# Kernel tuning notes

Hardware: AMD Instinct MI355X
Metric: run time of the kernel (lower is better)

The kernel has to match this reference:

```python
import jax, jax.numpy as jnp
import numpy as np

N = 100000
E = 1600000
D_IN = 128
D_H = 128


def _logit(p):
    p = max(min(p, 0.999), 0.001)
    return float(np.log(p / (1.0 - p)))


def setup_inputs() -> dict:
    key = jax.random.key(0)
    ks = jax.random.split(key, 16)
    s = 0.05
    inp = {
        "x": jax.random.normal(ks[0], (N, D_IN), jnp.float32),
        "edge_index": jax.random.randint(ks[1], (2, E), 0, N, jnp.int64),
        "reranker_scores": jax.random.normal(ks[2], (N,), jnp.float32),
        # input_proj
        "Wp": jax.random.normal(ks[3], (D_IN, D_H), jnp.float32) * s,
        "bp": jnp.zeros((D_H,), jnp.float32),
        # SAGEConv 0: lin_l (on aggregated neighbors, has bias), lin_r (root, no bias)
        "Wl0": jax.random.normal(ks[4], (D_IN, D_H), jnp.float32) * s,
        "bl0": jnp.zeros((D_H,), jnp.float32),
        "Wr0": jax.random.normal(ks[5], (D_IN, D_H), jnp.float32) * s,
        # SAGEConv 1
        "Wl1": jax.random.normal(ks[6], (D_H, D_H), jnp.float32) * s,
        "bl1": jnp.zeros((D_H,), jnp.float32),
        "Wr1": jax.random.normal(ks[7], (D_H, D_H), jnp.float32) * s,
        # score head: Linear(128,64) -> GELU -> Linear(64,1)
        "Ws1": jax.random.normal(ks[8], (D_H, D_H // 2), jnp.float32) * s,
        "bs1": jnp.zeros((D_H // 2,), jnp.float32),
        "Ws2": jax.random.normal(ks[9], (D_H // 2, 1), jnp.float32) * s,
        "bs2": jnp.zeros((1,), jnp.float32),
        "alpha_logit": jnp.asarray(_logit(0.65), jnp.float32),
    }
    return inp


def _sage(h, src, dst, Wl, bl, Wr):
    # PyG SAGEConv (aggr='mean'): lin_l(mean_{j in N(i)} x_j) + lin_r(x_i)
    agg = jax.ops.segment_sum(h[src], dst, num_segments=N)  # [N, d]
    deg = jax.ops.segment_sum(jnp.ones((src.shape[0],), h.dtype), dst, num_segments=N)
    mean = agg / jnp.maximum(deg, 1.0)[:, None]
    return mean @ Wl + bl + h @ Wr


def reference(x, edge_index, reranker_scores, Wp, bp, Wl0, bl0, Wr0, Wl1, bl1, Wr1,
              Ws1, bs1, Ws2, bs2, alpha_logit):
    src, dst = edge_index[0], edge_index[1]
    gelu = lambda t: jax.nn.gelu(t, approximate=False)  # torch nn.GELU default = exact erf
    residual = x @ Wp + bp
    # layer 0 (dropout inactive at eval)
    h = gelu(_sage(x, src, dst, Wl0, bl0, Wr0)) + residual
    # layer 1
    h = gelu(_sage(h, src, dst, Wl1, bl1, Wr1)) + h
    gnn_scores = (gelu(h @ Ws1 + bs1) @ Ws2 + bs2)[:, 0]  # [N]
    alpha = jax.nn.sigmoid(alpha_logit)
    return alpha * reranker_scores + (1.0 - alpha) * gnn_scores
```

## Files before the change

kernel.cpp:

```cpp
#include <hip/hip_runtime.h>

typedef unsigned short u16;
typedef unsigned char  u8;
typedef unsigned int   u32;
typedef unsigned long long u64;
typedef __attribute__((ext_vector_type(8))) short short8;
typedef __attribute__((ext_vector_type(4))) float f32x4;
typedef __attribute__((ext_vector_type(2))) float f32x2;

#define PIN8(v) asm volatile("" : "+v"(v))

__device__ __forceinline__ float b2f(u16 u) { return __uint_as_float(((u32)u) << 16); }
__device__ __forceinline__ u16 f2b(float f) {
    u32 i = __float_as_uint(f);
    return (u16)((i + 0x7FFFu + ((i >> 16) & 1u)) >> 16);
}
__device__ __forceinline__ float gelu_f(float v) {
    return 0.5f * v * (1.f + erff(v * 0.70710678118654752f));
}
__device__ __forceinline__ float ldf(const void* p, int i, int f32) {
    return f32 ? ((const float*)p)[i] : b2f(((const u16*)p)[i]);
}

__device__ __forceinline__ float fp8_dec(u32 v) {
    u32 bits = ((v & 0x80u) << 24) | ((v & 0x7Fu) << 20);
    return __uint_as_float(bits) * 1.3292279957849159e36f;
}
__device__ __forceinline__ u32 fp8_enc(float x) {
    u32 b = __float_as_uint(x);
    u32 s = (b >> 24) & 0x80u;
    float ax = fminf(__uint_as_float(b & 0x7FFFFFFFu), 448.f);
    u32 r;
    if (ax < 0.015625f) {
        r = (u32)(ax * 512.f + 0.5f);
    } else {
        u32 ab = __float_as_uint(ax);
        u32 rb = ab + 0x7FFFFu + ((ab >> 20) & 1u);
        int e8 = (int)(rb >> 23) - 120;
        u32 m = (rb >> 20) & 7u;
        if (e8 > 15) { e8 = 15; m = 6u; }
        r = ((u32)e8 << 3) | m;
    }
    return s | r;
}

__device__ __forceinline__ f32x2 dec2_fp8(u32 v) {
#if __has_builtin(__builtin_amdgcn_cvt_pk_f32_fp8)
    return __builtin_amdgcn_cvt_pk_f32_fp8((int)v, false);
#else
    f32x2 r; r[0] = fp8_dec(v); r[1] = fp8_dec(v >> 8); return r;
#endif
}
__device__ __forceinline__ u32 pk4_fp8(float v0, float v1, float v2, float v3) {
#if __has_builtin(__builtin_amdgcn_cvt_pk_fp8_f32)
    int p = __builtin_amdgcn_cvt_pk_fp8_f32(v0, v1, 0, false);
    p = __builtin_amdgcn_cvt_pk_fp8_f32(v2, v3, p, true);
    return (u32)p;
#else
    return fp8_enc(v0) | (fp8_enc(v1) << 8) | (fp8_enc(v2) << 16) | (fp8_enc(v3) << 24);
#endif
}

__global__ void probe_kernel(const int* __restrict__ ei, const u16* __restrict__ xw,
                             int* __restrict__ mode) {
    int lane = threadIdx.x;
    int v = (lane < 8) ? ei[2 * lane + 1] : 0;
    unsigned long long nz = __ballot(v != 0);
    u16 h = xw[2 * lane];
    int e = (h >> 7) & 0xFF;
    unsigned long long pl = __ballot(e >= 100 && e <= 140);
    if (lane == 0) {
        mode[0] = (nz == 0ULL) ? 1 : 0;
        mode[1] = (__popcll(pl) >= 48) ? 0 : 1;
    }
}

__global__ __launch_bounds__(256) void fallback_kernel(const void* __restrict__ rr,
                                                       const void* __restrict__ al,
                                                       const int* __restrict__ mode,
                                                       void* __restrict__ out, int N) {
    int i = blockIdx.x * 256 + threadIdx.x;
    if (i >= N) return;
    int f32 = mode ? mode[1] : 0;
    float a = 1.f / (1.f + expf(-ldf(al, 0, f32)));
    float v = a * ldf(rr, i, f32);
    if (f32) ((float*)out)[i] = v; else ((u16*)out)[i] = f2b(v);
}

__global__ __launch_bounds__(256) void hist_kernel(const int* __restrict__ ei, int E, int N,
                                                   const int* __restrict__ mode,
                                                   int* __restrict__ deg) {
    int i = blockIdx.x * 256 + threadIdx.x;
    if (i >= E) return;
    int m64 = mode[0];
    int d = m64 ? ei[2 * E + 2 * i] : ei[E + i];
    if ((unsigned)d < (unsigned)N) atomicAdd(&deg[d], 1);
}

__global__ __launch_bounds__(256) void bucketHist2_kernel(const int* __restrict__ ei, int E, int N,
                                                          const int* __restrict__ mode, int shift,
                                                          int* __restrict__ chist, int chunks) {
    __shared__ int h[1024];
    int t = threadIdx.x;
#pragma unroll
    for (int j = 0; j < 4; j++) h[t + j * 256] = 0;
    __syncthreads();
    const int m64 = mode[0];
    const int base = blockIdx.x * 2048;
#pragma unroll
    for (int j = 0; j < 8; j++) {
        int i = base + j * 256 + t;
        if (i < E) {
            int d = m64 ? ei[2 * E + 2 * i] : ei[E + i];
            if ((unsigned)d < (unsigned)N) atomicAdd(&h[d >> shift], 1);
        }
    }
    __syncthreads();
#pragma unroll
    for (int j = 0; j < 4; j++) {
        int b = t + j * 256;
        chist[(size_t)b * chunks + blockIdx.x] = h[b];
    }
}

__global__ __launch_bounds__(256) void scanA_kernel(const int* __restrict__ deg,
                                                    int* __restrict__ part) {
    int t = threadIdx.x, lane = t & 63, wv = t >> 6;
    size_t base = (size_t)blockIdx.x * 2048 + (size_t)t * 8;
    int s = 0;
#pragma unroll
    for (int j = 0; j < 8; j++) s += deg[base + j];
    for (int m = 1; m < 64; m <<= 1) s += __shfl_xor(s, m, 64);
    __shared__ int ws4[4];
    if (lane == 0) ws4[wv] = s;
    __syncthreads();
    if (t == 0) part[blockIdx.x] = ws4[0] + ws4[1] + ws4[2] + ws4[3];
}

__global__ void scanB_kernel(int* __restrict__ part, int nb) {
    int lane = threadIdx.x;
    int v = (lane < nb) ? part[lane] : 0;
    int orig = v;
    for (int d = 1; d < 64; d <<= 1) {
        int o = __shfl_up(v, d, 64);
        if (lane >= d) v += o;
    }
    if (lane < nb) part[lane] = v - orig;
}

__global__ __launch_bounds__(256) void scanC_kernel(const int* __restrict__ deg,
                                                    const int* __restrict__ part,
                                                    int* __restrict__ off) {
    int t = threadIdx.x, lane = t & 63, wv = t >> 6;
    size_t base = (size_t)blockIdx.x * 2048 + (size_t)t * 8;
    int v[8];
    int s = 0;
#pragma unroll
    for (int j = 0; j < 8; j++) { v[j] = deg[base + j]; s += v[j]; }
    int incl = s;
    for (int d = 1; d < 64; d <<= 1) {
        int o = __shfl_up(incl, d, 64);
        if (lane >= d) incl += o;
    }
    __shared__ int wsum[4];
    if (lane == 63) wsum[wv] = incl;
    __syncthreads();
    int pre = part[blockIdx.x] + (incl - s);
    for (int w = 0; w < wv; w++) pre += wsum[w];
#pragma unroll
    for (int j = 0; j < 8; j++) { off[base + j] = pre; pre += v[j]; }
    if (blockIdx.x == gridDim.x - 1 && t == 255) off[base + 8] = pre;
}

__global__ __launch_bounds__(256) void scanK_kernel(const int* __restrict__ bcnt,
                                                    int* __restrict__ boff) {
    int t = threadIdx.x, lane = t & 63, wv = t >> 6;
    int v[4];
    int s = 0;
#pragma unroll
    for (int j = 0; j < 4; j++) { v[j] = bcnt[t * 4 + j]; s += v[j]; }
    int incl = s;
    for (int d = 1; d < 64; d <<= 1) {
        int o = __shfl_up(incl, d, 64);
        if (lane >= d) incl += o;
    }
    __shared__ int wsum[4];
    if (lane == 63) wsum[wv] = incl;
    __syncthreads();
    int pre = incl - s;
    for (int w = 0; w < wv; w++) pre += wsum[w];
#pragma unroll
    for (int j = 0; j < 4; j++) { boff[t * 4 + j] = pre; pre += v[j]; }
    if (t == 255) boff[1024] = pre;
}

__global__ __launch_bounds__(256) void chunkScanPre_kernel(int* __restrict__ chist,
                                                           int* __restrict__ bcnt, int chunks) {
    const int b = (blockIdx.x * 256 + threadIdx.x) >> 6;
    if (b >= 1024) return;
    const int lane = threadIdx.x & 63;
    const int per = (chunks + 63) >> 6;
    int* row = chist + (size_t)b * chunks;
    int v[32];
    int sum = 0;
#pragma unroll
    for (int j = 0; j < 32; j++) {
        int c = lane * per + j;
        v[j] = (j < per && c < chunks) ? row[c] : 0;
        sum += v[j];
    }
    int pre = sum;
    for (int d = 1; d < 64; d <<= 1) {
        int o = __shfl_up(pre, d, 64);
        if (lane >= d) pre += o;
    }
    if (lane == 63) bcnt[b] = pre;
    pre -= sum;
#pragma unroll
    for (int j = 0; j < 32; j++) {
        int c = lane * per + j;
        if (j < per && c < chunks) { row[c] = pre; pre += v[j]; }
    }
}

__global__ __launch_bounds__(256) void bucketScatter2_kernel(const int* __restrict__ ei, int E, int N,
                                                             const int* __restrict__ mode, int shift,
                                                             const int* __restrict__ cbase,
                                                             const int* __restrict__ boff,
                                                             u64* __restrict__ pairs, int chunks) {
    __shared__ int cur[1024];
    int t = threadIdx.x;
#pragma unroll
    for (int j = 0; j < 4; j++) {
        int b = t + j * 256;
        cur[b] = cbase[(size_t)b * chunks + blockIdx.x] + boff[b];
    }
    __syncthreads();
    const int m64 = mode[0];
    const int base = blockIdx.x * 2048;
#pragma unroll
    for (int j = 0; j < 8; j++) {
        int i = base + j * 256 + t;
        if (i < E) {
            int d = m64 ? ei[2 * E + 2 * i] : ei[E + i];
            if ((unsigned)d >= (unsigned)N) continue;
            int s = m64 ? ei[2 * i] : ei[i];
            if ((unsigned)s >= (unsigned)N) s = 0;
            int p = atomicAdd(&cur[d >> shift], 1);
            pairs[p] = ((u64)(u32)d << 32) | (u32)s;
        }
    }
}

__global__ __launch_bounds__(256) void bucketFill2_kernel(const u64* __restrict__ pairs,
                                                          const int* __restrict__ boff,
                                                          int* __restrict__ off,
                                                          int* __restrict__ sorted,
                                                          int shift, int E, int N) {
    __shared__ int cur[2048];
    __shared__ int wsum[4];
    const int b = blockIdx.x;
    const int t = threadIdx.x;
    const int lane = t & 63, wv = t >> 6;
    const int nodes = 1 << shift;
    const int nbase = b << shift;
    for (int i = t; i < nodes; i += 256) cur[i] = 0;
    __syncthreads();
    const int s0 = boff[b], s1 = boff[b + 1];
    for (int i = s0 + t; i < s1; i += 256) {
        int li = (int)(pairs[i] >> 32) - nbase;
        if ((unsigned)li < (unsigned)nodes) atomicAdd(&cur[li], 1);
    }
    __syncthreads();
    const int per = (nodes + 255) >> 8;
    int v[8];
    int sum = 0;
#pragma unroll
    for (int j = 0; j < 8; j++) {
        int idx = t * per + j;
        v[j] = (j < per && idx < nodes) ? cur[idx] : 0;
        sum += v[j];
    }
    int incl = sum;
    for (int d = 1; d < 64; d <<= 1) {
        int o = __shfl_up(incl, d, 64);
        if (lane >= d) incl += o;
    }
    if (lane == 63) wsum[wv] = incl;
    __syncthreads();
    int pre = s0 + (incl - sum);
    for (int w = 0; w < wv; w++) pre += wsum[w];
#pragma unroll
    for (int j = 0; j < 8; j++) {
        int idx = t * per + j;
        if (j < per && idx < nodes) {
            cur[idx] = pre;
            if (nbase + idx <= N) off[nbase + idx] = pre;
            pre += v[j];
        }
    }
    if (t == 255 && nbase + nodes <= N) off[nbase + nodes] = s1;
    __syncthreads();
    for (int i = s0 + t; i < s1; i += 256) {
        u64 pr = pairs[i];
        int li = (int)(pr >> 32) - nbase;
        if ((unsigned)li >= (unsigned)nodes) continue;
        int p = atomicAdd(&cur[li], 1);
        if ((unsigned)p < (unsigned)E) sorted[p] = (int)(u32)pr;
    }
}

__global__ __launch_bounds__(256) void fill_kernel(const int* __restrict__ ei, int E, int N,
                                                   const int* __restrict__ mode,
                                                   const int* __restrict__ off,
                                                   int* __restrict__ deg,
                                                   int* __restrict__ sorted) {
    int i = blockIdx.x * 256 + threadIdx.x;
    if (i >= E) return;
    int m64 = mode[0];
    int s = m64 ? ei[2 * i] : ei[i];
    int d = m64 ? ei[2 * E + 2 * i] : ei[E + i];
    if ((unsigned)d >= (unsigned)N) return;
    if ((unsigned)s >= (unsigned)N) s = 0;
    int p = atomicSub(&deg[d], 1) - 1;
    if (p < 0) return;
    int pos = off[d] + p;
    if ((unsigned)pos < (unsigned)E) sorted[pos] = s;
}

__global__ __launch_bounds__(256) void prep_kernel(const void* __restrict__ Wp, const void* __restrict__ Wl0,
                                                   const void* __restrict__ Wr0, const void* __restrict__ Wl1,
                                                   const void* __restrict__ Wr1, const void* __restrict__ Ws1,
                                                   const int* __restrict__ mode, u16* __restrict__ T) {
    int idx = blockIdx.x * 256 + threadIdx.x;
    int f32 = mode[1];
    if (idx < 81920) {
        int m = idx >> 14, e = idx & 16383, n = e & 127, k = e >> 7;
        const void* s;
        switch (m) {
            case 0: s = Wp; break;
            case 1: s = Wl0; break;
            case 2: s = Wr0; break;
            case 3: s = Wl1; break;
            default: s = Wr1; break;
        }
        T[m * 16384 + n * 128 + k] = f2b(ldf(s, e, f32));
    } else if (idx < 90112) {
        int e = idx - 81920, k = e >> 6, n = e & 63;
        T[81920 + n * 128 + k] = f2b(ldf(Ws1, e, f32));
    }
}

template <int F32>
__global__ __launch_bounds__(256) void cvt8_kernel(const void* __restrict__ H, u8* __restrict__ F,
                                                   const int* __restrict__ mode, int NE, int checkMode) {
    if (checkMode && mode[1] != F32) return;
    int i = blockIdx.x * 256 + threadIdx.x;
    if (i >= NE) return;
    float x0, x1;
    if (!F32) {
        u32 v = ((const u32*)H)[i];
        x0 = b2f((u16)v); x1 = b2f((u16)(v >> 16));
    } else {
        x0 = ((const float*)H)[2 * i]; x1 = ((const float*)H)[2 * i + 1];
    }
#if __has_builtin(__builtin_amdgcn_cvt_pk_fp8_f32)
    ((u16*)F)[i] = (u16)__builtin_amdgcn_cvt_pk_fp8_f32(x0, x1, 0, false);
#else
    ((u16*)F)[i] = (u16)(fp8_enc(x0) | (fp8_enc(x1) << 8));
#endif
}

__global__ __launch_bounds__(256) void sagg8_kernel(const u8* __restrict__ F, const int* __restrict__ off,
                                                    const int* __restrict__ srcs, u16* __restrict__ meanO,
                                                    int N, int E) {
    const int node = __builtin_amdgcn_readfirstlane(blockIdx.x * 4 + (threadIdx.x >> 6));
    if (node >= N) return;
    const int lane = threadIdx.x & 63;
    int s0 = off[node], s1 = off[node + 1];
    if (s0 < 0) s0 = 0;
    if (s1 > E) s1 = E;
    if (s1 < s0) s1 = s0;
    const int dg = s1 - s0;
    const float inv = 1.f / (float)(dg > 1 ? dg : 1);
    const u8* Fp = F + lane * 2;
    float a0 = 0.f, a1 = 0.f;
    for (int base = s0; base < s1; base += 64) {
        const int rem = s1 - base;
        const int cnt = rem < 64 ? rem : 64;
        int msrc = srcs[base + (lane < cnt ? lane : 0)];
        if ((unsigned)msrc >= (unsigned)N) msrc = 0;
        int e = 0;
        for (; e + 7 < cnt; e += 8) {
            int i0 = __shfl(msrc, e + 0, 64);
            int i1 = __shfl(msrc, e + 1, 64);
            int i2 = __shfl(msrc, e + 2, 64);
            int i3 = __shfl(msrc, e + 3, 64);
            int i4 = __shfl(msrc, e + 4, 64);
            int i5 = __shfl(msrc, e + 5, 64);
            int i6 = __shfl(msrc, e + 6, 64);
            int i7 = __shfl(msrc, e + 7, 64);
            u32 v0 = *(const u16*)(Fp + (size_t)i0 * 128);
            u32 v1 = *(const u16*)(Fp + (size_t)i1 * 128);
            u32 v2 = *(const u16*)(Fp + (size_t)i2 * 128);
            u32 v3 = *(const u16*)(Fp + (size_t)i3 * 128);
            u32 v4 = *(const u16*)(Fp + (size_t)i4 * 128);
            u32 v5 = *(const u16*)(Fp + (size_t)i5 * 128);
            u32 v6 = *(const u16*)(Fp + (size_t)i6 * 128);
            u32 v7 = *(const u16*)(Fp + (size_t)i7 * 128);
            f32x2 d0 = dec2_fp8(v0), d1 = dec2_fp8(v1), d2 = dec2_fp8(v2), d3 = dec2_fp8(v3);
            f32x2 d4 = dec2_fp8(v4), d5 = dec2_fp8(v5), d6 = dec2_fp8(v6), d7 = dec2_fp8(v7);
            a0 += (d0[0] + d1[0]) + (d2[0] + d3[0]) + (d4[0] + d5[0]) + (d6[0] + d7[0]);
            a1 += (d0[1] + d1[1]) + (d2[1] + d3[1]) + (d4[1] + d5[1]) + (d6[1] + d7[1]);
        }
        for (; e + 3 < cnt; e += 4) {
            int i0 = __shfl(msrc, e + 0, 64);
            int i1 = __shfl(msrc, e + 1, 64);
            int i2 = __shfl(msrc, e + 2, 64);
            int i3 = __shfl(msrc, e + 3, 64);
            u32 v0 = *(const u16*)(Fp + (size_t)i0 * 128);
            u32 v1 = *(const u16*)(Fp + (size_t)i1 * 128);
            u32 v2 = *(const u16*)(Fp + (size_t)i2 * 128);
            u32 v3 = *(const u16*)(Fp + (size_t)i3 * 128);
            f32x2 d0 = dec2_fp8(v0), d1 = dec2_fp8(v1), d2 = dec2_fp8(v2), d3 = dec2_fp8(v3);
            a0 += (d0[0] + d1[0]) + (d2[0] + d3[0]);
            a1 += (d0[1] + d1[1]) + (d2[1] + d3[1]);
        }
        for (; e < cnt; ++e) {
            int i0 = __shfl(msrc, e, 64);
            f32x2 d0 = dec2_fp8(*(const u16*)(Fp + (size_t)i0 * 128));
            a0 += d0[0];
            a1 += d0[1];
        }
    }
    *(u32*)(meanO + (size_t)node * 128 + lane * 2) = (u32)f2b(a0 * inv) | ((u32)f2b(a1 * inv) << 16);
}

template <int F32>
__global__ __launch_bounds__(256) void saggb_kernel(const void* __restrict__ H, const int* __restrict__ off,
                                                    const int* __restrict__ srcs, u16* __restrict__ meanO,
                                                    int N, int E, const int* __restrict__ mode, int mcheck) {
    if (mcheck && mode[1] != F32) return;
    const int node = __builtin_amdgcn_readfirstlane(blockIdx.x * 4 + (threadIdx.x >> 6));
    if (node >= N) return;
    const int lane = threadIdx.x & 63;
    int s0 = off[node], s1 = off[node + 1];
    if (s0 < 0) s0 = 0;
    if (s1 > E) s1 = E;
    if (s1 < s0) s1 = s0;
    const int dg = s1 - s0;
    const float inv = 1.f / (float)(dg > 1 ? dg : 1);
    float a0 = 0.f, a1 = 0.f;
    if (!F32) {
        const u32* Hp = (const u32*)H + lane;
        for (int e = s0; e < s1; ++e) {
            int i0 = srcs[e];
            if ((unsigned)i0 >= (unsigned)N) i0 = 0;
            u32 v0 = Hp[(size_t)i0 << 6];
            a0 += __uint_as_float(v0 << 16);
            a1 += __uint_as_float(v0 & 0xFFFF0000u);
        }
    } else {
        const float* Hp = (const float*)H + 2 * lane;
        for (int e = s0; e < s1; ++e) {
            int i0 = srcs[e];
            if ((unsigned)i0 >= (unsigned)N) i0 = 0;
            const float2 w0 = *(const float2*)(Hp + ((size_t)i0 << 7));
            a0 += w0.x;
            a1 += w0.y;
        }
    }
    *(u32*)(meanO + (size_t)node * 128 + lane * 2) = (u32)f2b(a0 * inv) | ((u32)f2b(a1 * inv) << 16);
}

__device__ __forceinline__ uint4 packbf8(f32x4 a, f32x4 b) {
    uint4 o;
    o.x = (u32)f2b(a[0]) | ((u32)f2b(a[1]) << 16);
    o.y = (u32)f2b(a[2]) | ((u32)f2b(a[3]) << 16);
    o.z = (u32)f2b(b[0]) | ((u32)f2b(b[1]) << 16);
    o.w = (u32)f2b(b[2]) | ((u32)f2b(b[3]) << 16);
    return o;
}

template <int F32>
__device__ __forceinline__ void stageTile(const void* __restrict__ src, u16* __restrict__ lds,
                                          long tb, int N, int t) {
    const int r = t >> 2;
    long gr = tb + r;
    if (gr >= N) gr = N - 1;
    const int cb = (t & 3) * 64;
    const int swz = (r & 7) << 4;
    char* lp = (char*)lds + r * 256;
    if (!F32) {
        const char* gp = (const char*)src + gr * 256 + cb;
        uint4 v0 = *(const uint4*)(gp + 0);
        uint4 v1 = *(const uint4*)(gp + 16);
        uint4 v2 = *(const uint4*)(gp + 32);
        uint4 v3 = *(const uint4*)(gp + 48);
        *(uint4*)(lp + ((cb + 0) ^ swz)) = v0;
        *(uint4*)(lp + ((cb + 16) ^ swz)) = v1;
        *(uint4*)(lp + ((cb + 32) ^ swz)) = v2;
        *(uint4*)(lp + ((cb + 48) ^ swz)) = v3;
    } else {
        const float* gp = (const float*)src + gr * 128 + (cb >> 1);
        f32x4 f[8];
#pragma unroll
        for (int j = 0; j < 8; j++) f[j] = *(const f32x4*)(gp + 4 * j);
#pragma unroll
        for (int j = 0; j < 4; j++)
            *(uint4*)(lp + ((cb + 16 * j) ^ swz)) = packbf8(f[2 * j], f[2 * j + 1]);
    }
}

template <int F32>
__device__ __forceinline__ void stageTileA(const void* __restrict__ src, u16* __restrict__ lds,
                                           long tb, int N, int t) {
    const int r = t >> 2;
    long gr = tb + r;
    if (gr >= N) gr = N - 1;
    const int cb = (t & 3) * 64;
    const int swz = (r & 15) << 4;
    char* lp = (char*)lds + r * 256;
    if (!F32) {
        const char* gp = (const char*)src + gr * 256 + cb;
        uint4 v0 = *(const uint4*)(gp + 0);
        uint4 v1 = *(const uint4*)(gp + 16);
        uint4 v2 = *(const uint4*)(gp + 32);
        uint4 v3 = *(const uint4*)(gp + 48);
        *(uint4*)(lp + ((cb + 0) ^ swz)) = v0;
        *(uint4*)(lp + ((cb + 16) ^ swz)) = v1;
        *(uint4*)(lp + ((cb + 32) ^ swz)) = v2;
        *(uint4*)(lp + ((cb + 48) ^ swz)) = v3;
    } else {
        const float* gp = (const float*)src + gr * 128 + (cb >> 1);
        f32x4 f[8];
#pragma unroll
        for (int j = 0; j < 8; j++) f[j] = *(const f32x4*)(gp + 4 * j);
#pragma unroll
        for (int j = 0; j < 4; j++)
            *(uint4*)(lp + ((cb + 16 * j) ^ swz)) = packbf8(f[2 * j], f[2 * j + 1]);
    }
}

template <int F32>
__global__ __launch_bounds__(256, 2) void gemmF_kernel(const void* __restrict__ x, const u16* __restrict__ mean,
                                                       const u16* __restrict__ WTl, const u16* __restrict__ WTr,
                                                       const u16* __restrict__ WTp,
                                                       const void* __restrict__ bl, const void* __restrict__ bp,
                                                       const int* __restrict__ mode,
                                                       u16* __restrict__ h0, u8* __restrict__ F8, int emitF8,
                                                       int N) {
    if (mode[1] != F32) return;
    __shared__ u16 lsW[3 * 64 * 128];
    __shared__ u16 lsA[2 * 64 * 128];
    const int t = threadIdx.x;
    const int lane = t & 63, wave = t >> 6;
    const int m0 = lane & 15, q = lane >> 4;
    const int nh = blockIdx.x & 1;
    const int rg = blockIdx.x >> 1;

#pragma unroll
    for (int m = 0; m < 3; m++) {
        const u16* Wm = (m == 0) ? WTl : (m == 1) ? WTr : WTp;
#pragma unroll
        for (int j = 0; j < 4; j++) {
            int c = t + j * 256;
            int nrow = c >> 4, cb = (c & 15) * 16;
            short8 v = *(const short8*)(Wm + (size_t)(nh * 64 + nrow) * 128 + (cb >> 1));
            *(short8*)((char*)lsW + m * 16384 + nrow * 256 + (cb ^ ((nrow & 15) << 4))) = v;
        }
    }

    const int colg = nh * 4 + wave;
    const int wrow = wave * 16 + m0;
    const int wswz = m0 << 4;
    float blv[4], bpv[4];
#pragma unroll
    for (int g = 0; g < 4; g++) {
        const int col = colg * 16 + q * 4 + g;
        blv[g] = ldf(bl, col, F32);
        bpv[g] = ldf(bp, col, F32);
    }

    const long tiles = ((long)N + 63) >> 6;
    for (long tile = rg; tile < tiles; tile += 256) {
        const long tb = tile * 64;
        stageTileA<0>(mean, lsA, tb, N, t);
        stageTileA<F32>(x, lsA + 64 * 128, tb, N, t);
        __syncthreads();

        f32x4 accU[4], accR[4];
#pragma unroll
        for (int rt = 0; rt < 4; rt++) { accU[rt] = {0.f, 0.f, 0.f, 0.f}; accR[rt] = {0.f, 0.f, 0.f, 0.f}; }

#pragma unroll
        for (int ks = 0; ks < 4; ks++) {
            const int kb = ks * 64 + q * 16;
            short8 wlF = *(const short8*)((char*)lsW + 0 * 16384 + wrow * 256 + (kb ^ wswz));
            short8 wrF = *(const short8*)((char*)lsW + 1 * 16384 + wrow * 256 + (kb ^ wswz));
            short8 wpF = *(const short8*)((char*)lsW + 2 * 16384 + wrow * 256 + (kb ^ wswz));
#pragma unroll
            for (int rt = 0; rt < 4; rt++) {
                const int ab = (rt * 16 + m0) * 256 + (kb ^ (m0 << 4));
                short8 aM = *(const short8*)((char*)lsA + ab);
                short8 aX = *(const short8*)((char*)lsA + 16384 + ab);
                accU[rt] = __builtin_amdgcn_mfma_f32_16x16x32_bf16(wlF, aM, accU[rt], 0, 0, 0);
                accU[rt] = __builtin_amdgcn_mfma_f32_16x16x32_bf16(wrF, aX, accU[rt], 0, 0, 0);
                accR[rt] = __builtin_amdgcn_mfma_f32_16x16x32_bf16(wpF, aX, accR[rt], 0, 0, 0);
            }
        }

#pragma unroll
        for (int rt = 0; rt < 4; rt++) {
            const long row = tb + rt * 16 + m0;
            if (row < N) {
                float v[4];
#pragma unroll
                for (int g = 0; g < 4; g++)
                    v[g] = gelu_f(accU[rt][g] + blv[g]) + accR[rt][g] + bpv[g];
                const int col0 = colg * 16 + q * 4;
                u64 pk = (u64)f2b(v[0]) | ((u64)f2b(v[1]) << 16) | ((u64)f2b(v[2]) << 32) | ((u64)f2b(v[3]) << 48);
                *(u64*)(h0 + (size_t)row * 128 + col0) = pk;
                if (emitF8)
                    *(u32*)(F8 + (size_t)row * 128 + col0) = pk4_fp8(v[0], v[1], v[2], v[3]);
            }
        }
        __syncthreads();
    }
}

__global__ __launch_bounds__(256, 2) void gemm1_kernel(const u16* __restrict__ h0, const u16* mean,
                                                       const u16* __restrict__ WTl, const u16* __restrict__ WTr,
                                                       const void* __restrict__ bl, const int* __restrict__ mode,
                                                       u16* h1, int N) {
    __shared__ u16 lsM[64 * 128];
    __shared__ u16 lsH[64 * 128];
    const int t = threadIdx.x;
    const int lane = t & 63, wave = t >> 6;
    const int m0 = lane & 15, q = lane >> 4;
    const int f32 = mode[1];
    const long tb = (long)blockIdx.x * 64;

    short8 wl[4][2], wr[4][2];
#pragma unroll
    for (int ks = 0; ks < 4; ks++)
#pragma unroll
        for (int h = 0; h < 2; h++) {
            const int ro = ((2 * wave + h) * 16 + m0) * 128 + ks * 32 + q * 8;
            wl[ks][h] = *(const short8*)(WTl + ro);
            wr[ks][h] = *(const short8*)(WTr + ro);
        }
#pragma unroll
    for (int ks = 0; ks < 4; ks++)
#pragma unroll
        for (int h = 0; h < 2; h++) { PIN8(wl[ks][h]); PIN8(wr[ks][h]); }

    stageTile<0>(mean, lsM, tb, N, t);
    stageTile<0>(h0, lsH, tb, N, t);
    __syncthreads();

    f32x4 acc[4][2];
#pragma unroll
    for (int rt = 0; rt < 4; rt++)
#pragma unroll
        for (int h = 0; h < 2; h++) acc[rt][h] = {0.f, 0.f, 0.f, 0.f};

    const int swz = (m0 & 7) << 4;
#pragma unroll
    for (int ks = 0; ks < 4; ks++) {
        short8 aM[4], aH[4];
#pragma unroll
        for (int rt = 0; rt < 4; rt++) {
            const int off = (rt * 16 + m0) * 256 + ((ks * 64 + q * 16) ^ swz);
            aM[rt] = *(const short8*)((const char*)lsM + off);
            aH[rt] = *(const short8*)((const char*)lsH + off);
        }
#pragma unroll
        for (int rt = 0; rt < 4; rt++)
#pragma unroll
            for (int h = 0; h < 2; h++) {
                acc[rt][h] = __builtin_amdgcn_mfma_f32_16x16x32_bf16(wl[ks][h], aM[rt], acc[rt][h], 0, 0, 0);
                acc[rt][h] = __builtin_amdgcn_mfma_f32_16x16x32_bf16(wr[ks][h], aH[rt], acc[rt][h], 0, 0, 0);
            }
    }

    float blv[2][4];
#pragma unroll
    for (int h = 0; h < 2; h++)
#pragma unroll
        for (int g = 0; g < 4; g++) blv[h][g] = ldf(bl, (2 * wave + h) * 16 + q * 4 + g, f32);

#pragma unroll
    for (int rt = 0; rt < 4; rt++) {
        const long row = tb + rt * 16 + m0;
        if (row < N) {
#pragma unroll
            for (int h = 0; h < 2; h++) {
                const int col0 = (2 * wave + h) * 16 + q * 4;
                const int rb = (rt * 16 + m0) * 256 + (((2 * wave + h) * 32 + q * 8) ^ swz);
                const u64 old = *(const u64*)((const char*)lsH + rb);
                float v[4];
#pragma unroll
                for (int g = 0; g < 4; g++)
                    v[g] = gelu_f(acc[rt][h][g] + blv[h][g]) + b2f((u16)(old >> (16 * g)));
                u64 pk = (u64)f2b(v[0]) | ((u64)f2b(v[1]) << 16) | ((u64)f2b(v[2]) << 32) | ((u64)f2b(v[3]) << 48);
                *(u64*)(h1 + (size_t)row * 128 + col0) = pk;
            }
        }
    }
}

__global__ __launch_bounds__(256, 4) void score_kernel(const u16* __restrict__ h1, const u16* __restrict__ WTs,
                                                       const void* __restrict__ bs1, const void* __restrict__ w2,
                                                       const void* __restrict__ bs2, const void* __restrict__ rr,
                                                       const void* __restrict__ alpha_p, const int* __restrict__ mode,
                                                       void* __restrict__ out, int N) {
    const int lane = threadIdx.x & 63, wave = threadIdx.x >> 6;
    const int m0 = lane & 15, q = lane >> 4;
    const int f32 = mode[1];
    const long rowBase = (long)blockIdx.x * 128 + wave * 32;
    f32x4 acc[2][4];
#pragma unroll
    for (int r = 0; r < 2; r++)
#pragma unroll
        for (int n = 0; n < 4; n++) acc[r][n] = {0.f, 0.f, 0.f, 0.f};
#pragma unroll
    for (int ks = 0; ks < 4; ++ks) {
        const int k = ks * 32 + q * 8;
        short8 bf[4];
#pragma unroll
        for (int n = 0; n < 4; n++) bf[n] = *(const short8*)(WTs + (n * 16 + m0) * 128 + k);
#pragma unroll
        for (int r = 0; r < 2; r++) {
            long row = rowBase + r * 16 + m0;
            if (row >= N) row = N - 1;
            short8 a = *(const short8*)(h1 + (size_t)row * 128 + k);
#pragma unroll
            for (int n = 0; n < 4; n++)
                acc[r][n] = __builtin_amdgcn_mfma_f32_16x16x32_bf16(a, bf[n], acc[r][n], 0, 0, 0);
        }
    }
    float alpha = 1.f / (1.f + expf(-ldf(alpha_p, 0, f32)));
    float bs2v = ldf(bs2, 0, f32);
    float w2v[4], b1v[4];
#pragma unroll
    for (int n = 0; n < 4; n++) {
        int col = n * 16 + m0;
        w2v[n] = ldf(w2, col, f32);
        b1v[n] = ldf(bs1, col, f32);
    }
#pragma unroll
    for (int r = 0; r < 2; r++) {
        float s[4] = {0.f, 0.f, 0.f, 0.f};
#pragma unroll
        for (int n = 0; n < 4; n++)
#pragma unroll
            for (int g = 0; g < 4; g++) s[g] += gelu_f(acc[r][n][g] + b1v[n]) * w2v[n];
#pragma unroll
        for (int g = 0; g < 4; g++) {
            s[g] += __shfl_xor(s[g], 1, 64);
            s[g] += __shfl_xor(s[g], 2, 64);
            s[g] += __shfl_xor(s[g], 4, 64);
            s[g] += __shfl_xor(s[g], 8, 64);
        }
        if (m0 == 0) {
            long row0 = rowBase + r * 16 + q * 4;
#pragma unroll
            for (int g = 0; g < 4; g++) {
                long row = row0 + g;
                if (row < N) {
                    float sc = s[g] + bs2v;
                    float v = alpha * ldf(rr, (int)row, f32) + (1.f - alpha) * sc;
                    if (f32) ((float*)out)[row] = v; else ((u16*)out)[row] = f2b(v);
                }
            }
        }
    }
}

extern "C" void kernel_launch(void* const* d_in, const int* in_sizes, int n_in,
                              void* d_out, int out_size, void* d_ws, size_t ws_size,
                              hipStream_t stream) {
    const void* x = d_in[0];
    const int* ei = (const int*)d_in[1];
    const void* rr = d_in[2];
    const void* Wp = d_in[3];
    const void* bp = d_in[4];
    const void* Wl0 = d_in[5];
    const void* bl0 = d_in[6];
    const void* Wr0 = d_in[7];
    const void* Wl1 = d_in[8];
    const void* bl1 = d_in[9];
    const void* Wr1 = d_in[10];
    const void* Ws1 = d_in[11];
    const void* bs1 = d_in[12];
    const void* Ws2 = d_in[13];
    const void* bs2 = d_in[14];
    const void* alpha = d_in[15];

    const int N = in_sizes[0] / 128;
    const int E = in_sizes[1] / 2;
    const int NP = ((N + 2047) / 2048) * 2048;
    const int NB = NP / 2048;
    const int chunks = (E + 2047) / 2048;
    int shift = 0;
    while (((N - 1) >> shift) >= 1024) shift++;

    char* w = (char*)d_ws;
    size_t used = 0;
    auto alloc = [&](size_t b) { char* p = w + used; used += (b + 255) & ~(size_t)255; return p; };
    int* mode = (int*)alloc(256);
    int* deg = (int*)alloc((size_t)NP * 4);
    int* bcnt = (int*)alloc(1024 * 4);
    int* boff = (int*)alloc(1025 * 4);
    int* chist = (int*)alloc((size_t)chunks * 1024 * 4);
    int* off = (int*)alloc((size_t)(NP + 64) * 4);
    int* part = (int*)alloc(64 * 4);
    int* sorted = (int*)alloc((size_t)E * 4);
    u16* T = (u16*)alloc(90112 * 2);
    u16* meanb = (u16*)alloc((size_t)NP * 128 * 2);
    u16* h0 = (u16*)alloc((size_t)NP * 128 * 2);
    u16* h1 = meanb;
    size_t usedBase = used;
    size_t fbytes = (size_t)NP * 128;
    if ((size_t)E * 8 > fbytes) fbytes = (size_t)E * 8;
    u8* F = (u8*)alloc(fbytes);
    size_t usedFull = used;
    u64* pairs = (u64*)F;

    if (ws_size < 4096) {
        fallback_kernel<<<(N + 255) / 256, 256, 0, stream>>>(rr, alpha, nullptr, d_out, N);
        return;
    }
    probe_kernel<<<1, 64, 0, stream>>>(ei, (const u16*)x, mode);
    if (usedBase > ws_size) {
        fallback_kernel<<<(N + 255) / 256, 256, 0, stream>>>(rr, alpha, mode, d_out, N);
        return;
    }
    const bool fp8Path = (usedFull <= ws_size);
    const bool bucketPath = fp8Path && ((1 << shift) <= 2048) && (chunks <= 2048);

    prep_kernel<<<(90112 + 255) / 256, 256, 0, stream>>>(Wp, Wl0, Wr0, Wl1, Wr1, Ws1, mode, T);

    if (bucketPath) {
        bucketHist2_kernel<<<chunks, 256, 0, stream>>>(ei, E, N, mode, shift, chist, chunks);
        chunkScanPre_kernel<<<256, 256, 0, stream>>>(chist, bcnt, chunks);
        scanK_kernel<<<1, 256, 0, stream>>>(bcnt, boff);
        bucketScatter2_kernel<<<chunks, 256, 0, stream>>>(ei, E, N, mode, shift, chist, boff, pairs, chunks);
        bucketFill2_kernel<<<1024, 256, 0, stream>>>(pairs, boff, off, sorted, shift, E, N);
    } else {
        hipMemsetAsync(deg, 0, (size_t)NP * 4, stream);
        hist_kernel<<<(E + 255) / 256, 256, 0, stream>>>(ei, E, N, mode, deg);
        scanA_kernel<<<NB, 256, 0, stream>>>(deg, part);
        scanB_kernel<<<1, 64, 0, stream>>>(part, NB);
        scanC_kernel<<<NB, 256, 0, stream>>>(deg, part, off);
        fill_kernel<<<(E + 255) / 256, 256, 0, stream>>>(ei, E, N, mode, off, deg, sorted);
    }

    const int gemmGrid16 = (N + 63) / 64;
    const int nodeBlocks = (N + 3) / 4;
    const int NE = N * 64;
    const int cvtGrid = (NE + 255) / 256;

    if (fp8Path) {
        cvt8_kernel<0><<<cvtGrid, 256, 0, stream>>>(x, F, mode, NE, 1);
        cvt8_kernel<1><<<cvtGrid, 256, 0, stream>>>(x, F, mode, NE, 1);
        sagg8_kernel<<<nodeBlocks, 256, 0, stream>>>(F, off, sorted, meanb, N, E);
        gemmF_kernel<0><<<512, 256, 0, stream>>>(x, meanb, T + 16384, T + 32768, T + 0, bl0, bp, mode, h0, F, 1, N);
        gemmF_kernel<1><<<512, 256, 0, stream>>>(x, meanb, T + 16384, T + 32768, T + 0, bl0, bp, mode, h0, F, 1, N);
        sagg8_kernel<<<nodeBlocks, 256, 0, stream>>>(F, off, sorted, meanb, N, E);
    } else {
        saggb_kernel<0><<<nodeBlocks, 256, 0, stream>>>(x, off, sorted, meanb, N, E, mode, 1);
        saggb_kernel<1><<<nodeBlocks, 256, 0, stream>>>(x, off, sorted, meanb, N, E, mode, 1);
        gemmF_kernel<0><<<512, 256, 0, stream>>>(x, meanb, T + 16384, T + 32768, T + 0, bl0, bp, mode, h0, nullptr, 0, N);
        gemmF_kernel<1><<<512, 256, 0, stream>>>(x, meanb, T + 16384, T + 32768, T + 0, bl0, bp, mode, h0, nullptr, 0, N);
        saggb_kernel<0><<<nodeBlocks, 256, 0, stream>>>(h0, off, sorted, meanb, N, E, mode, 0);
    }
    gemm1_kernel<<<gemmGrid16, 256, 0, stream>>>(h0, meanb, T + 49152, T + 65536, bl1, mode, h1, N);
    score_kernel<<<(N + 127) / 128, 256, 0, stream>>>(h1, T + 81920, bs1, Ws2, bs2, rr, alpha, mode, d_out, N);
}
```

Measured before the change: 353.7 us.

## Gather four neighbor rows per wave with 8-byte loads in fp8 aggregation

Reworks the fp8 mean-aggregation kernel so each wave splits into four 16-lane groups. Each group loads a whole 128-byte fp8 neighbor row using 8-byte loads per lane, instead of every lane loading 2 bytes from the same row. Partial sums are combined with cross-lane xor shuffles, and one group writes the result with a 16-byte store. The aim is fewer, wider memory instructions and more rows in flight per wave. In exchange it adds 8 accumulators per lane, a reduction step, and a per-edge shuffle with a branch in place of the old unrolled batches.

```diff
diff --git a/kernel.cpp b/kernel.cpp
--- a/kernel.cpp
+++ b/kernel.cpp
@@ -49,6 +49,15 @@
     return __builtin_amdgcn_cvt_pk_f32_fp8((int)v, false);
 #else
     f32x2 r; r[0] = fp8_dec(v); r[1] = fp8_dec(v >> 8); return r;
+#endif
+}
+__device__ __forceinline__ void dec4_fp8(u32 v, float* o) {
+#if __has_builtin(__builtin_amdgcn_cvt_pk_f32_fp8)
+    f32x2 lo = __builtin_amdgcn_cvt_pk_f32_fp8((int)v, false);
+    f32x2 hi = __builtin_amdgcn_cvt_pk_f32_fp8((int)v, true);
+    o[0] = lo[0]; o[1] = lo[1]; o[2] = hi[0]; o[3] = hi[1];
+#else
+    o[0] = fp8_dec(v); o[1] = fp8_dec(v >> 8); o[2] = fp8_dec(v >> 16); o[3] = fp8_dec(v >> 24);
 #endif
 }
 __device__ __forceinline__ u32 pk4_fp8(float v0, float v1, float v2, float v3) {
@@ -377,63 +386,48 @@
     const int node = __builtin_amdgcn_readfirstlane(blockIdx.x * 4 + (threadIdx.x >> 6));
     if (node >= N) return;
     const int lane = threadIdx.x & 63;
+    const int rep = lane >> 4;
+    const int cl = lane & 15;
     int s0 = off[node], s1 = off[node + 1];
     if (s0 < 0) s0 = 0;
     if (s1 > E) s1 = E;
     if (s1 < s0) s1 = s0;
     const int dg = s1 - s0;
     const float inv = 1.f / (float)(dg > 1 ? dg : 1);
-    const u8* Fp = F + lane * 2;
-    float a0 = 0.f, a1 = 0.f;
+    float a[8];
+#pragma unroll
+    for (int j = 0; j < 8; j++) a[j] = 0.f;
     for (int base = s0; base < s1; base += 64) {
         const int rem = s1 - base;
         const int cnt = rem < 64 ? rem : 64;
         int msrc = srcs[base + (lane < cnt ? lane : 0)];
         if ((unsigned)msrc >= (unsigned)N) msrc = 0;
-        int e = 0;
-        for (; e + 7 < cnt; e += 8) {
-            int i0 = __shfl(msrc, e + 0, 64);
-            int i1 = __shfl(msrc, e + 1, 64);
-            int i2 = __shfl(msrc, e + 2, 64);
-            int i3 = __shfl(msrc, e + 3, 64);
-            int i4 = __shfl(msrc, e + 4, 64);
-            int i5 = __shfl(msrc, e + 5, 64);
-            int i6 = __shfl(msrc, e + 6, 64);
-            int i7 = __shfl(msrc, e + 7, 64);
-            u32 v0 = *(const u16*)(Fp + (size_t)i0 * 128);
-            u32 v1 = *(const u16*)(Fp + (size_t)i1 * 128);
-            u32 v2 = *(const u16*)(Fp + (size_t)i2 * 128);
-            u32 v3 = *(const u16*)(Fp + (size_t)i3 * 128);
-            u32 v4 = *(const u16*)(Fp + (size_t)i4 * 128);
-            u32 v5 = *(const u16*)(Fp + (size_t)i5 * 128);
-            u32 v6 = *(const u16*)(Fp + (size_t)i6 * 128);
-            u32 v7 = *(const u16*)(Fp + (size_t)i7 * 128);
-            f32x2 d0 = dec2_fp8(v0), d1 = dec2_fp8(v1), d2 = dec2_fp8(v2), d3 = dec2_fp8(v3);
-            f32x2 d4 = dec2_fp8(v4), d5 = dec2_fp8(v5), d6 = dec2_fp8(v6), d7 = dec2_fp8(v7);
-            a0 += (d0[0] + d1[0]) + (d2[0] + d3[0]) + (d4[0] + d5[0]) + (d6[0] + d7[0]);
-            a1 += (d0[1] + d1[1]) + (d2[1] + d3[1]) + (d4[1] + d5[1]) + (d6[1] + d7[1]);
-        }
-        for (; e + 3 < cnt; e += 4) {
-            int i0 = __shfl(msrc, e + 0, 64);
-            int i1 = __shfl(msrc, e + 1, 64);
-            int i2 = __shfl(msrc, e + 2, 64);
-            int i3 = __shfl(msrc, e + 3, 64);
-            u32 v0 = *(const u16*)(Fp + (size_t)i0 * 128);
-            u32 v1 = *(const u16*)(Fp + (size_t)i1 * 128);
-            u32 v2 = *(const u16*)(Fp + (size_t)i2 * 128);
-            u32 v3 = *(const u16*)(Fp + (size_t)i3 * 128);
-            f32x2 d0 = dec2_fp8(v0), d1 = dec2_fp8(v1), d2 = dec2_fp8(v2), d3 = dec2_fp8(v3);
-            a0 += (d0[0] + d1[0]) + (d2[0] + d3[0]);
-            a1 += (d0[1] + d1[1]) + (d2[1] + d3[1]);
-        }
-        for (; e < cnt; ++e) {
-            int i0 = __shfl(msrc, e, 64);
-            f32x2 d0 = dec2_fp8(*(const u16*)(Fp + (size_t)i0 * 128));
-            a0 += d0[0];
-            a1 += d0[1];
-        }
-    }
-    *(u32*)(meanO + (size_t)node * 128 + lane * 2) = (u32)f2b(a0 * inv) | ((u32)f2b(a1 * inv) << 16);
+        for (int e = 0; e < cnt; e += 4) {
+            const int er = e + rep;
+            int isrc = __shfl(msrc, er, 64);
+            if (er < cnt) {
+                u64 v = *(const u64*)(F + (size_t)isrc * 128 + cl * 8);
+                float d0[4], d1[4];
+                dec4_fp8((u32)v, d0);
+                dec4_fp8((u32)(v >> 32), d1);
+                a[0] += d0[0]; a[1] += d0[1]; a[2] += d0[2]; a[3] += d0[3];
+                a[4] += d1[0]; a[5] += d1[1]; a[6] += d1[2]; a[7] += d1[3];
+            }
+        }
+    }
+#pragma unroll
+    for (int j = 0; j < 8; j++) {
+        a[j] += __shfl_xor(a[j], 16, 64);
+        a[j] += __shfl_xor(a[j], 32, 64);
+    }
+    if (rep == 0) {
+        uint4 o;
+        o.x = (u32)f2b(a[0] * inv) | ((u32)f2b(a[1] * inv) << 16);
+        o.y = (u32)f2b(a[2] * inv) | ((u32)f2b(a[3] * inv) << 16);
+        o.z = (u32)f2b(a[4] * inv) | ((u32)f2b(a[5] * inv) << 16);
+        o.w = (u32)f2b(a[6] * inv) | ((u32)f2b(a[7] * inv) << 16);
+        *(uint4*)(meanO + (size_t)node * 128 + cl * 8) = o;
+    }
 }
 
 template <int F32>
```

New measurement: 365.8 us. 1.03x slower.
